# Kernel optimization log

Hardware: AMD Instinct MI355X
Metric: run time of the kernel (lower is better)

The kernel has to match this reference:

```python
import jax, jax.numpy as jnp
import numpy as np

B, D, N, H = 2, 1024, 2048, 16
Da = D // H
NEG = -1e30


def setup_inputs() -> dict:
    key = jax.random.key(0)
    k1, k2, k3, k4, k5 = jax.random.split(key, 5)
    x = jax.random.normal(k1, (B, D, N), dtype=jnp.float32)
    mask = jnp.ones((B, N), dtype=jnp.float32)
    s = 1.0 / np.sqrt(D)
    Wq = jax.random.normal(k2, (H, D, Da), dtype=jnp.float32) * s
    Wk = jax.random.normal(k3, (H, D, Da), dtype=jnp.float32) * s
    Wv = jax.random.normal(k4, (H, D, Da), dtype=jnp.float32) * s
    Wo = jax.random.normal(k5, (D, D), dtype=jnp.float32) * s
    return {"x": x, "mask": mask, "Wq": Wq, "Wk": Wk, "Wv": Wv, "Wo": Wo}


def reference(x, mask, Wq, Wk, Wv, Wo):
    # x: [B, D, N] -> [B, N, D]
    xt = jnp.swapaxes(x, 1, 2)
    scale = 1.0 / np.sqrt(Da)
    # per-head projections, batched over heads: [B, H, N, Da]
    q = jnp.einsum("bnd,hde->bhne", xt, Wq)
    k = jnp.einsum("bnd,hde->bhne", xt, Wk)
    v = jnp.einsum("bnd,hde->bhne", xt, Wv)
    # scaled scores: [B, H, N, N]
    scores = jnp.einsum("bhne,bhme->bhnm", q, k) * scale
    hmask = mask[:, None, None, :]  # additive mask over keys
    vmask = mask[:, None, :, None]  # multiplicative mask over queries
    scores = scores * hmask + (1.0 - hmask) * NEG
    attn = jax.nn.softmax(scores, axis=-1) * vmask
    heads = jnp.einsum("bhnm,bhme->bhne", attn, v)
    # concat heads along feature dim: [B, N, H*Da]
    head = jnp.swapaxes(heads, 1, 2).reshape(xt.shape[0], xt.shape[1], H * Da)
    out = head @ Wo  # [B, N, D]
    return jnp.swapaxes(out, 1, 2)  # [B, D, N]
```

## Files before the change

### kernel.cpp

```cpp
#include <hip/hip_runtime.h>

typedef _Float16 f16;
typedef _Float16 f16x4 __attribute__((ext_vector_type(4)));
typedef _Float16 f16x8 __attribute__((ext_vector_type(8)));
typedef __fp16 fp16x2 __attribute__((ext_vector_type(2)));
typedef float f32x4 __attribute__((ext_vector_type(4)));
typedef float f32x16 __attribute__((ext_vector_type(16)));
typedef int i32x4 __attribute__((ext_vector_type(4)));

#define NEGV (-1e30f)
#define MBASE 10.0f

#if __has_builtin(__builtin_amdgcn_exp2f)
#define EXP2(x) __builtin_amdgcn_exp2f(x)
#else
#define EXP2(x) exp2f(x)
#endif

__device__ __forceinline__ void gload16(const f16* g, f16* l) {
  __builtin_amdgcn_global_load_lds(
      (const __attribute__((address_space(1))) void*)g,
      (__attribute__((address_space(3))) void*)l, 16, 0, 0);
}

__device__ __forceinline__ int pkh(float a, float b) {
  fp16x2 p = __builtin_amdgcn_cvt_pkrtz(a, b);
  return __builtin_bit_cast(int, p);
}

__device__ __forceinline__ void plswap(int& a, int& b) {
#if __has_builtin(__builtin_amdgcn_permlane32_swap)
  auto r = __builtin_amdgcn_permlane32_swap(a, b, false, false);
  a = r[0];
  b = r[1];
#else
  int an = __shfl_xor(b, 32);
  int bn = __shfl_xor(a, 32);
  bool lo = (threadIdx.x & 63) < 32;
  int a2 = lo ? a : an;
  int b2 = lo ? bn : b;
  a = a2;
  b = b2;
#endif
}

__global__ __launch_bounds__(256) void prep_kernel(
    const float* __restrict__ x, const float* __restrict__ Wq,
    const float* __restrict__ Wk, const float* __restrict__ Wv,
    const float* __restrict__ Wo, f16* __restrict__ xt,
    f16* __restrict__ WqkvT, f16* __restrict__ WoT)
{
  __shared__ float t[32][33];
  int tx = threadIdx.x & 31, ty = threadIdx.x >> 5;
  int id = blockIdx.x;
  const float* src;
  f16* dst;
  int a0, b0, sld;
  float sc = 1.0f;
  if (id < 4096) {
    int b = id >> 11, rem = id & 2047;
    a0 = (rem >> 6) * 32;
    b0 = (rem & 63) * 32;
    sld = 2048;
    src = x + (size_t)b * 1024 * 2048;
    dst = xt + (size_t)b * 2048 * 1024;
  } else if (id < 7168) {
    int i = id - 4096;
    a0 = (i & 31) * 32;
    b0 = ((i >> 5) & 1) * 32;
    int z = i >> 6, m = z >> 4, h = z & 15;
    sld = 64;
    src = ((m == 0) ? Wq : (m == 1) ? Wk : Wv) + (size_t)h * 65536;
    sc = (m == 0) ? 0.18033688011112042f : 1.0f;
    dst = WqkvT + (size_t)(m * 1024 + h * 64) * 1024;
  } else {
    int i = id - 7168;
    a0 = (i >> 5) * 32;
    b0 = (i & 31) * 32;
    sld = 1024;
    src = Wo;
    dst = WoT;
  }
#pragma unroll
  for (int i = 0; i < 4; ++i)
    t[ty + 8 * i][tx] = src[(size_t)(a0 + ty + 8 * i) * sld + b0 + tx] * sc;
  __syncthreads();
#pragma unroll
  for (int i = 0; i < 4; ++i)
    dst[(size_t)(b0 + ty + 8 * i) * 1024 + a0 + tx] = (f16)t[tx][ty + 8 * i];
}

template <int BN>
__global__ __launch_bounds__(512, 4) void gemm_f16_kernel(
    const f16* __restrict__ A, const f16* __restrict__ Bt,
    int K, int ldc, long bstride, long cstride,
    f16* __restrict__ Ch, float* __restrict__ Cf,
    const float* __restrict__ rowmask, int mcol0,
    f16* __restrict__ Vt)
{
  const int NACC = BN / 64;
  __shared__ __align__(16) f16 smem[16384];
  f16* As = smem;
  f16* Bs = smem + 8192;

  int tid = threadIdx.x;
  int lane = tid & 63, w = tid >> 6, g = lane >> 4, r = lane & 15;
  int wr = w >> 2, wc = w & 3;

  int nbx = gridDim.x;
  int n = nbx * gridDim.y;
  int flat = blockIdx.y * nbx + blockIdx.x;
  int nf = (flat & 7) * (n >> 3) + (flat >> 3);
  int bx = nf % nbx, by = nf / nbx;

  size_t row0 = (size_t)by * 128;
  size_t col0 = (size_t)bx * BN;
  Bt += (size_t)blockIdx.z * (size_t)bstride;

  int l8 = lane >> 3;
  int sseg = ((lane & 7) ^ l8) * 8;
  int r7 = r & 7;

  f32x4 acc[4][NACC];
#pragma unroll
  for (int m = 0; m < 4; ++m)
#pragma unroll
    for (int nn = 0; nn < NACC; ++nn)
      acc[m][nn] = (f32x4){0.f, 0.f, 0.f, 0.f};

  const f16* Ap = A + (row0 + w * 16 + l8) * (size_t)K + sseg;
  const f16* Bp;
  if (BN == 128)
    Bp = Bt + (col0 + w * 16 + l8) * (size_t)K + sseg;
  else
    Bp = Bt + (col0 + w * 8 + l8) * (size_t)K + sseg;

  for (int k0 = 0; k0 < K; k0 += 64) {
    __syncthreads();
#pragma unroll
    for (int i = 0; i < 2; ++i)
      gload16(Ap + (size_t)i * 8 * K + k0, As + w * 1024 + i * 512);
    if (BN == 128) {
#pragma unroll
      for (int i = 0; i < 2; ++i)
        gload16(Bp + (size_t)i * 8 * K + k0, Bs + w * 1024 + i * 512);
    } else {
      gload16(Bp + k0, Bs + w * 512);
    }
    __syncthreads();
#pragma unroll
    for (int j = 0; j < 2; ++j) {
      f16x8 af[4], bf[NACC];
      int tseg = j * 4 + g;
#pragma unroll
      for (int m = 0; m < 4; ++m)
        af[m] = *(const f16x8*)&As[(wr * 64 + m * 16 + r) * 64 + ((tseg ^ r7) << 3)];
#pragma unroll
      for (int nn = 0; nn < NACC; ++nn) {
        int brow = (BN == 128) ? (wc * 32 + nn * 16 + r) : (wc * 16 + r);
        bf[nn] = *(const f16x8*)&Bs[brow * 64 + ((tseg ^ r7) << 3)];
      }
#pragma unroll
      for (int m = 0; m < 4; ++m)
#pragma unroll
        for (int nn = 0; nn < NACC; ++nn)
          acc[m][nn] = __builtin_amdgcn_mfma_f32_16x16x32_f16(af[m], bf[nn], acc[m][nn], 0, 0, 0);
    }
  }

  if (BN == 128 && Vt && col0 >= 2048) {
    int b = (int)(row0 >> 11);
    int n0 = (int)(row0 & 2047);
    int vcol0 = (int)col0 - 2048;
    __syncthreads();
#pragma unroll
    for (int h2 = 0; h2 < 2; ++h2) {
      if ((wc >> 1) == h2) {
        int wcl = wc & 1;
#pragma unroll
        for (int m = 0; m < 4; ++m)
#pragma unroll
          for (int nn = 0; nn < NACC; ++nn) {
            int cl = wcl * 32 + nn * 16 + r;
            int row = wr * 64 + m * 16 + g * 4;
            int rowp = row ^ ((cl & 7) << 3);
            f16x4 v4 = {(f16)acc[m][nn][0], (f16)acc[m][nn][1],
                        (f16)acc[m][nn][2], (f16)acc[m][nn][3]};
            *(f16x4*)&smem[cl * 128 + rowp] = v4;
          }
      }
      __syncthreads();
#pragma unroll
      for (int ii = 0; ii < 2; ++ii) {
        int chunk = ii * 512 + tid;
        int el = chunk >> 4, seg = chunk & 15;
        int rowp = (seg * 8) ^ ((el & 7) << 3);
        f16x8 v8 = *(const f16x8*)&smem[el * 128 + rowp];
        *(f16x8*)&Vt[(size_t)(b * 1024 + vcol0 + h2 * 64 + el) * 2048 + n0 + seg * 8] = v8;
      }
      __syncthreads();
    }
  } else if (Ch) {
    Ch += (size_t)blockIdx.z * (size_t)cstride;
#pragma unroll
    for (int m = 0; m < 4; ++m)
#pragma unroll
      for (int nn = 0; nn < NACC; ++nn)
#pragma unroll
        for (int q = 0; q < 4; ++q) {
          size_t row = row0 + wr * 64 + m * 16 + g * 4 + q;
          int col = (int)col0 + ((BN == 128) ? (wc * 32 + nn * 16 + r) : (wc * 16 + r));
          float v = acc[m][nn][q];
          if (rowmask && col >= mcol0) v *= rowmask[row];
          Ch[row * (size_t)ldc + col] = (f16)v;
        }
  } else {
    Cf += (size_t)blockIdx.z * (size_t)cstride;
#pragma unroll
    for (int m = 0; m < 4; ++m)
#pragma unroll
      for (int nn = 0; nn < NACC; ++nn)
#pragma unroll
        for (int q = 0; q < 4; ++q) {
          int col = (int)col0 + ((BN == 128) ? (wc * 32 + nn * 16 + r) : (wc * 16 + r));
          Cf[(row0 + wr * 64 + m * 16 + g * 4 + q) * (size_t)ldc + col] = acc[m][nn][q];
        }
  }
}

__global__ __launch_bounds__(512, 4) void attn_kernel(const f16* __restrict__ qk,
                                                      const f16* __restrict__ Vt,
                                                      const float* __restrict__ mask,
                                                      f16* __restrict__ head)
{
  __shared__ __align__(16) f16 smem[32768];
  __shared__ __align__(16) float negc[2048];
  __shared__ __align__(16) float ll[8][32];
  __shared__ __align__(16) float il[4][32];
  __shared__ int aflag;

  int tid = threadIdx.x;
  int w = tid >> 6, lane = tid & 63;
  int l31 = lane & 31, hb = lane >> 5;
  int hb4 = hb * 4;
  int wq = w >> 1, wk = w & 1;

  int flat = blockIdx.x;
  int nf = (flat & 7) * 64 + (flat >> 3);
  int qt = nf & 15, bh = nf >> 4;
  int b = bh >> 4, hh = bh & 15;
  const float* maskb = mask + b * 2048;

  if (tid == 0) aflag = 0;

  int qrow = qt * 128 + wq * 32 + l31;
  const f16* qp = qk + ((size_t)(b * 2048 + qrow)) * 2048 + hh * 64;
  f16x8 qf[4];
#pragma unroll
  for (int ec = 0; ec < 4; ++ec)
    qf[ec] = *(const f16x8*)(qp + ec * 16 + hb * 8);

  const f16* kg0 = qk + ((size_t)(b * 2048)) * 2048 + 1024 + hh * 64;
  const f16* vg0 = Vt + ((size_t)((b * 16 + hh) * 64)) * 2048;

  int ksrow = tid >> 3, kseg = tid & 7;
  int ks2 = (kseg ^ (ksrow & 7)) * 8;
  int vsrow = tid >> 4, vseg2 = tid & 15;
  int vs2 = (vseg2 ^ (vsrow & 7)) * 8;

  auto stage = [&](int nb, int kt_) {
    const f16* kg = kg0 + (size_t)kt_ * 128 * 2048;
    const f16* vg = vg0 + kt_ * 128;
    f16* Kd = smem + nb * 8192;
    f16* Vd = smem + 16384 + nb * 8192;
    gload16(kg + (size_t)ksrow * 2048 + ks2, Kd + w * 512);
    gload16(kg + (size_t)(ksrow + 64) * 2048 + ks2, Kd + 4096 + w * 512);
    gload16(vg + (size_t)vsrow * 2048 + vs2, Vd + w * 512);
    gload16(vg + (size_t)(vsrow + 32) * 2048 + vs2, Vd + 4096 + w * 512);
  };

  stage(0, 0);
  __syncthreads();

  {
    const float* mp = maskb + tid * 4;
    f32x4 m0 = *(const f32x4*)(mp);
    int localany = 0;
#pragma unroll
    for (int j = 0; j < 4; ++j) {
      negc[tid * 4 + j] = (1.0f - m0[j]) * NEGV;
      localany |= (m0[j] != 1.0f);
    }
    if (localany) aflag = 1;
  }
  __syncthreads();
  const bool anymask = (aflag != 0);

  f32x16 zc;
#pragma unroll
  for (int i = 0; i < 16; ++i) zc[i] = 0.f;
  f32x16 o0 = zc, o1 = zc;
  float lrun = 0.f;

  int kb0 = (wk * 64 + l31) * 64;
  int kb1 = kb0 + 2048;
  int k7 = l31 & 7;
  int vb0 = l31 * 128, vb1 = vb0 + 4096;

  for (int kt = 0; kt < 16; ++kt) {
    int cur = kt & 1;
    if (kt + 1 < 16) stage(cur ^ 1, kt + 1);

    const f16* Kc = smem + cur * 8192;
    const f16* Vc = smem + 16384 + cur * 8192;

    f32x16 c0 = zc, c1 = zc;
    if (anymask) {
      const float* nb = &negc[kt * 128 + wk * 64];
#pragma unroll
      for (int rr = 0; rr < 4; ++rr) {
        f32x4 cc0 = *(const f32x4*)&nb[rr * 8 + hb4];
        f32x4 cc1 = *(const f32x4*)&nb[32 + rr * 8 + hb4];
#pragma unroll
        for (int j = 0; j < 4; ++j) {
          c0[rr * 4 + j] = cc0[j];
          c1[rr * 4 + j] = cc1[j];
        }
      }
    }
    f32x16 s0, s1;
    __builtin_amdgcn_s_setprio(1);
    {
      int so = (((hb) ^ k7) << 3);
      f16x8 kf0 = *(const f16x8*)&Kc[kb0 + so];
      f16x8 kf1 = *(const f16x8*)&Kc[kb1 + so];
      s0 = __builtin_amdgcn_mfma_f32_32x32x16_f16(kf0, qf[0], c0, 0, 0, 0);
      s1 = __builtin_amdgcn_mfma_f32_32x32x16_f16(kf1, qf[0], c1, 0, 0, 0);
    }
#pragma unroll
    for (int ec = 1; ec < 4; ++ec) {
      int so = ((((ec << 1) | hb) ^ k7) << 3);
      f16x8 kf0 = *(const f16x8*)&Kc[kb0 + so];
      f16x8 kf1 = *(const f16x8*)&Kc[kb1 + so];
      s0 = __builtin_amdgcn_mfma_f32_32x32x16_f16(kf0, qf[ec], s0, 0, 0, 0);
      s1 = __builtin_amdgcn_mfma_f32_32x32x16_f16(kf1, qf[ec], s1, 0, 0, 0);
    }
    __builtin_amdgcn_s_setprio(0);

    float p[2][16];
#pragma unroll
    for (int i = 0; i < 16; ++i) {
      p[0][i] = EXP2(s0[i] - MBASE);
      p[1][i] = EXP2(s1[i] - MBASE);
    }
    float b2[16];
#pragma unroll
    for (int i = 0; i < 16; ++i) b2[i] = p[0][i] + p[1][i];
#pragma unroll
    for (int stp = 8; stp > 0; stp >>= 1)
#pragma unroll
      for (int i = 0; i < stp; ++i) b2[i] += b2[i + stp];
    lrun += b2[0];

    __builtin_amdgcn_s_setprio(1);
#pragma unroll
    for (int t = 0; t < 2; ++t)
#pragma unroll
      for (int kc = 0; kc < 2; ++kc) {
        int t0a = pkh(p[t][kc * 8 + 0], p[t][kc * 8 + 1]);
        int t0b = pkh(p[t][kc * 8 + 2], p[t][kc * 8 + 3]);
        int t1a = pkh(p[t][kc * 8 + 4], p[t][kc * 8 + 5]);
        int t1b = pkh(p[t][kc * 8 + 6], p[t][kc * 8 + 7]);
        plswap(t0a, t1a);
        plswap(t0b, t1b);
        f16x8 af = __builtin_bit_cast(f16x8, (i32x4){t0a, t0b, t1a, t1b});
        int vseg = wk * 8 + t * 4 + kc * 2 + hb;
        int vs = ((vseg ^ k7) << 3);
        f16x8 vf0 = *(const f16x8*)&Vc[vb0 + vs];
        f16x8 vf1 = *(const f16x8*)&Vc[vb1 + vs];
        o0 = __builtin_amdgcn_mfma_f32_32x32x16_f16(af, vf0, o0, 0, 0, 0);
        o1 = __builtin_amdgcn_mfma_f32_32x32x16_f16(af, vf1, o1, 0, 0, 0);
      }
    __builtin_amdgcn_s_setprio(0);

    __syncthreads();
  }

  lrun += __shfl_xor(lrun, 32);
  if (hb == 0) ll[w][l31] = lrun;
  __syncthreads();
  float lt = lrun + ll[w ^ 1][l31];
  if (wk == 0 && hb == 0) il[wq][l31] = maskb[qrow] / lt;
  float* scr = (float*)smem;
  if (wk == 1) {
    float* sp = scr + wq * 2048;
#pragma unroll
    for (int i = 0; i < 16; ++i) {
      sp[i * 64 + lane] = o0[i];
      sp[(16 + i) * 64 + lane] = o1[i];
    }
  }
  __syncthreads();
  if (wk == 0) {
    float* sp = scr + wq * 2048;
#pragma unroll
    for (int i = 0; i < 16; ++i) {
      o0[i] += sp[i * 64 + lane];
      o1[i] += sp[(16 + i) * 64 + lane];
    }
    f16* hp = head + ((size_t)(b * 2048 + qt * 128 + wq * 32)) * 1024 + hh * 64 + l31;
#pragma unroll
    for (int rr = 0; rr < 4; ++rr) {
      f32x4 iv = *(const f32x4*)&il[wq][rr * 8 + hb4];
#pragma unroll
      for (int j = 0; j < 4; ++j) {
        int crow = j + rr * 8 + hb4;
        hp[(size_t)crow * 1024] = (f16)(o0[rr * 4 + j] * iv[j]);
        hp[(size_t)crow * 1024 + 32] = (f16)(o1[rr * 4 + j] * iv[j]);
      }
    }
  }
}

extern "C" void kernel_launch(void* const* d_in, const int* in_sizes, int n_in,
                              void* d_out, int out_size, void* d_ws, size_t ws_size,
                              hipStream_t stream)
{
  const float* x    = (const float*)d_in[0];
  const float* mask = (const float*)d_in[1];
  const float* Wq   = (const float*)d_in[2];
  const float* Wk   = (const float*)d_in[3];
  const float* Wv   = (const float*)d_in[4];
  const float* Wo   = (const float*)d_in[5];
  float* out = (float*)d_out;

  char* ws = (char*)d_ws;
  f16* xt_head = (f16*)(ws);
  f16* WqkvT   = (f16*)(ws + 8388608);
  f16* WoT     = (f16*)(ws + 14680064);
  f16* qk      = (f16*)(ws + 16777216);
  f16* Vt      = (f16*)(ws + 33554432);

  prep_kernel<<<dim3(8192), 256, 0, stream>>>(x, Wq, Wk, Wv, Wo, xt_head, WqkvT, WoT);

  gemm_f16_kernel<128><<<dim3(24, 32, 1), 512, 0, stream>>>(
      xt_head, WqkvT, 1024, 2048, 0, 0, qk, nullptr, mask, 1024, Vt);

  attn_kernel<<<dim3(512), 512, 0, stream>>>(qk, Vt, mask, xt_head);

  gemm_f16_kernel<64><<<dim3(32, 8, 2), 512, 0, stream>>>(
      WoT, xt_head, 1024, 2048, (long)2048 * 1024, (long)1024 * 2048, nullptr, out,
      nullptr, 0, nullptr);
}
```

Baseline: 117.8 us.

## Halve attention query tile, drop LDS double buffering, split keys across four waves

The attention kernel now processes 64 query rows per block instead of 128, launches twice as many blocks, and splits each 128-key tile across four waves of 32 keys each instead of two waves of 64. K/V staging becomes single-buffered with a sync after each load, and the mask bias is stored as fp16. Together these cut LDS and register use so more blocks fit per CU (launch bounds raised to 8). The cost is that global-to-LDS loads no longer overlap compute, each K/V tile is reloaded by twice as many blocks, and the cross-wave output reduction needs extra LDS round trips. The mask constant changes from -1e30 to -60000 in fp16, which only matters when the mask contains zeros.

```diff
diff --git a/kernel.cpp b/kernel.cpp
--- a/kernel.cpp
+++ b/kernel.cpp
@@ -228,32 +228,45 @@
   }
 }
 
-__global__ __launch_bounds__(512, 4) void attn_kernel(const f16* __restrict__ qk,
+__global__ __launch_bounds__(512, 8) void attn_kernel(const f16* __restrict__ qk,
                                                       const f16* __restrict__ Vt,
                                                       const float* __restrict__ mask,
                                                       f16* __restrict__ head)
 {
-  __shared__ __align__(16) f16 smem[32768];
-  __shared__ __align__(16) float negc[2048];
+  __shared__ __align__(16) f16 smem[16384];
+  __shared__ __align__(16) f16 negcH[2048];
   __shared__ __align__(16) float ll[8][32];
-  __shared__ __align__(16) float il[4][32];
+  __shared__ __align__(16) float il[2][32];
   __shared__ int aflag;
 
   int tid = threadIdx.x;
   int w = tid >> 6, lane = tid & 63;
   int l31 = lane & 31, hb = lane >> 5;
   int hb4 = hb * 4;
-  int wq = w >> 1, wk = w & 1;
+  int wq = w >> 2, wk = w & 3;
 
   int flat = blockIdx.x;
-  int nf = (flat & 7) * 64 + (flat >> 3);
-  int qt = nf & 15, bh = nf >> 4;
+  int nf = (flat & 7) * 128 + (flat >> 3);
+  int qt = nf & 31, bh = nf >> 5;
   int b = bh >> 4, hh = bh & 15;
   const float* maskb = mask + b * 2048;
 
   if (tid == 0) aflag = 0;
-
-  int qrow = qt * 128 + wq * 32 + l31;
+  __syncthreads();
+
+  {
+    const float* mp = maskb + tid * 4;
+    f32x4 m0 = *(const f32x4*)(mp);
+    int localany = 0;
+#pragma unroll
+    for (int j = 0; j < 4; ++j) {
+      negcH[tid * 4 + j] = (f16)((1.0f - m0[j]) * -60000.0f);
+      localany |= (m0[j] != 1.0f);
+    }
+    if (localany) aflag = 1;
+  }
+
+  int qrow = qt * 64 + wq * 32 + l31;
   const f16* qp = qk + ((size_t)(b * 2048 + qrow)) * 2048 + hh * 64;
   f16x8 qf[4];
 #pragma unroll
@@ -268,31 +281,15 @@
   int vsrow = tid >> 4, vseg2 = tid & 15;
   int vs2 = (vseg2 ^ (vsrow & 7)) * 8;
 
-  auto stage = [&](int nb, int kt_) {
+  auto stage = [&](int kt_) {
     const f16* kg = kg0 + (size_t)kt_ * 128 * 2048;
     const f16* vg = vg0 + kt_ * 128;
-    f16* Kd = smem + nb * 8192;
-    f16* Vd = smem + 16384 + nb * 8192;
-    gload16(kg + (size_t)ksrow * 2048 + ks2, Kd + w * 512);
-    gload16(kg + (size_t)(ksrow + 64) * 2048 + ks2, Kd + 4096 + w * 512);
-    gload16(vg + (size_t)vsrow * 2048 + vs2, Vd + w * 512);
-    gload16(vg + (size_t)(vsrow + 32) * 2048 + vs2, Vd + 4096 + w * 512);
+    gload16(kg + (size_t)ksrow * 2048 + ks2, smem + w * 512);
+    gload16(kg + (size_t)(ksrow + 64) * 2048 + ks2, smem + 4096 + w * 512);
+    gload16(vg + (size_t)vsrow * 2048 + vs2, smem + 8192 + w * 512);
+    gload16(vg + (size_t)(vsrow + 32) * 2048 + vs2, smem + 12288 + w * 512);
   };
 
-  stage(0, 0);
-  __syncthreads();
-
-  {
-    const float* mp = maskb + tid * 4;
-    f32x4 m0 = *(const f32x4*)(mp);
-    int localany = 0;
-#pragma unroll
-    for (int j = 0; j < 4; ++j) {
-      negc[tid * 4 + j] = (1.0f - m0[j]) * NEGV;
-      localany |= (m0[j] != 1.0f);
-    }
-    if (localany) aflag = 1;
-  }
   __syncthreads();
   const bool anymask = (aflag != 0);
 
@@ -302,85 +299,63 @@
   f32x16 o0 = zc, o1 = zc;
   float lrun = 0.f;
 
-  int kb0 = (wk * 64 + l31) * 64;
-  int kb1 = kb0 + 2048;
+  int kb0 = (wk * 32 + l31) * 64;
   int k7 = l31 & 7;
   int vb0 = l31 * 128, vb1 = vb0 + 4096;
 
   for (int kt = 0; kt < 16; ++kt) {
-    int cur = kt & 1;
-    if (kt + 1 < 16) stage(cur ^ 1, kt + 1);
-
-    const f16* Kc = smem + cur * 8192;
-    const f16* Vc = smem + 16384 + cur * 8192;
-
-    f32x16 c0 = zc, c1 = zc;
+    stage(kt);
+    __syncthreads();
+
+    const f16* Kc = smem;
+    const f16* Vc = smem + 8192;
+
+    f32x16 s = zc;
     if (anymask) {
-      const float* nb = &negc[kt * 128 + wk * 64];
-#pragma unroll
-      for (int rr = 0; rr < 4; ++rr) {
-        f32x4 cc0 = *(const f32x4*)&nb[rr * 8 + hb4];
-        f32x4 cc1 = *(const f32x4*)&nb[32 + rr * 8 + hb4];
-#pragma unroll
-        for (int j = 0; j < 4; ++j) {
-          c0[rr * 4 + j] = cc0[j];
-          c1[rr * 4 + j] = cc1[j];
-        }
-      }
-    }
-    f32x16 s0, s1;
+      const f16* nb = &negcH[kt * 128 + wk * 32];
+#pragma unroll
+      for (int rr = 0; rr < 4; ++rr)
+#pragma unroll
+        for (int j = 0; j < 4; ++j)
+          s[rr * 4 + j] = (float)nb[rr * 8 + hb4 + j];
+    }
     __builtin_amdgcn_s_setprio(1);
-    {
-      int so = (((hb) ^ k7) << 3);
-      f16x8 kf0 = *(const f16x8*)&Kc[kb0 + so];
-      f16x8 kf1 = *(const f16x8*)&Kc[kb1 + so];
-      s0 = __builtin_amdgcn_mfma_f32_32x32x16_f16(kf0, qf[0], c0, 0, 0, 0);
-      s1 = __builtin_amdgcn_mfma_f32_32x32x16_f16(kf1, qf[0], c1, 0, 0, 0);
-    }
-#pragma unroll
-    for (int ec = 1; ec < 4; ++ec) {
+#pragma unroll
+    for (int ec = 0; ec < 4; ++ec) {
       int so = ((((ec << 1) | hb) ^ k7) << 3);
-      f16x8 kf0 = *(const f16x8*)&Kc[kb0 + so];
-      f16x8 kf1 = *(const f16x8*)&Kc[kb1 + so];
-      s0 = __builtin_amdgcn_mfma_f32_32x32x16_f16(kf0, qf[ec], s0, 0, 0, 0);
-      s1 = __builtin_amdgcn_mfma_f32_32x32x16_f16(kf1, qf[ec], s1, 0, 0, 0);
+      f16x8 kf = *(const f16x8*)&Kc[kb0 + so];
+      s = __builtin_amdgcn_mfma_f32_32x32x16_f16(kf, qf[ec], s, 0, 0, 0);
     }
     __builtin_amdgcn_s_setprio(0);
 
-    float p[2][16];
-#pragma unroll
-    for (int i = 0; i < 16; ++i) {
-      p[0][i] = EXP2(s0[i] - MBASE);
-      p[1][i] = EXP2(s1[i] - MBASE);
-    }
-    float b2[16];
-#pragma unroll
-    for (int i = 0; i < 16; ++i) b2[i] = p[0][i] + p[1][i];
-#pragma unroll
-    for (int stp = 8; stp > 0; stp >>= 1)
+#pragma unroll
+    for (int i = 0; i < 16; ++i) s[i] = EXP2(s[i] - MBASE);
+    float b2[8];
+#pragma unroll
+    for (int i = 0; i < 8; ++i) b2[i] = s[i] + s[i + 8];
+#pragma unroll
+    for (int stp = 4; stp > 0; stp >>= 1)
 #pragma unroll
       for (int i = 0; i < stp; ++i) b2[i] += b2[i + stp];
     lrun += b2[0];
 
     __builtin_amdgcn_s_setprio(1);
 #pragma unroll
-    for (int t = 0; t < 2; ++t)
-#pragma unroll
-      for (int kc = 0; kc < 2; ++kc) {
-        int t0a = pkh(p[t][kc * 8 + 0], p[t][kc * 8 + 1]);
-        int t0b = pkh(p[t][kc * 8 + 2], p[t][kc * 8 + 3]);
-        int t1a = pkh(p[t][kc * 8 + 4], p[t][kc * 8 + 5]);
-        int t1b = pkh(p[t][kc * 8 + 6], p[t][kc * 8 + 7]);
-        plswap(t0a, t1a);
-        plswap(t0b, t1b);
-        f16x8 af = __builtin_bit_cast(f16x8, (i32x4){t0a, t0b, t1a, t1b});
-        int vseg = wk * 8 + t * 4 + kc * 2 + hb;
-        int vs = ((vseg ^ k7) << 3);
-        f16x8 vf0 = *(const f16x8*)&Vc[vb0 + vs];
-        f16x8 vf1 = *(const f16x8*)&Vc[vb1 + vs];
-        o0 = __builtin_amdgcn_mfma_f32_32x32x16_f16(af, vf0, o0, 0, 0, 0);
-        o1 = __builtin_amdgcn_mfma_f32_32x32x16_f16(af, vf1, o1, 0, 0, 0);
-      }
+    for (int kc = 0; kc < 2; ++kc) {
+      int t0a = pkh(s[kc * 8 + 0], s[kc * 8 + 1]);
+      int t0b = pkh(s[kc * 8 + 2], s[kc * 8 + 3]);
+      int t1a = pkh(s[kc * 8 + 4], s[kc * 8 + 5]);
+      int t1b = pkh(s[kc * 8 + 6], s[kc * 8 + 7]);
+      plswap(t0a, t1a);
+      plswap(t0b, t1b);
+      f16x8 af = __builtin_bit_cast(f16x8, (i32x4){t0a, t0b, t1a, t1b});
+      int vseg = wk * 4 + kc * 2 + hb;
+      int vs = ((vseg ^ k7) << 3);
+      f16x8 vf0 = *(const f16x8*)&Vc[vb0 + vs];
+      f16x8 vf1 = *(const f16x8*)&Vc[vb1 + vs];
+      o0 = __builtin_amdgcn_mfma_f32_32x32x16_f16(af, vf0, o0, 0, 0, 0);
+      o1 = __builtin_amdgcn_mfma_f32_32x32x16_f16(af, vf1, o1, 0, 0, 0);
+    }
     __builtin_amdgcn_s_setprio(0);
 
     __syncthreads();
@@ -389,11 +364,13 @@
   lrun += __shfl_xor(lrun, 32);
   if (hb == 0) ll[w][l31] = lrun;
   __syncthreads();
-  float lt = lrun + ll[w ^ 1][l31];
-  if (wk == 0 && hb == 0) il[wq][l31] = maskb[qrow] / lt;
+  if (wk == 0 && hb == 0) {
+    float lt = ll[w][l31] + ll[w + 1][l31] + ll[w + 2][l31] + ll[w + 3][l31];
+    il[wq][l31] = maskb[qrow] / lt;
+  }
   float* scr = (float*)smem;
-  if (wk == 1) {
-    float* sp = scr + wq * 2048;
+  if (wk & 1) {
+    float* sp = scr + (wq * 2 + (wk >> 1)) * 2048;
 #pragma unroll
     for (int i = 0; i < 16; ++i) {
       sp[i * 64 + lane] = o0[i];
@@ -401,14 +378,32 @@
     }
   }
   __syncthreads();
-  if (wk == 0) {
-    float* sp = scr + wq * 2048;
+  if (!(wk & 1)) {
+    float* sp = scr + (wq * 2 + (wk >> 1)) * 2048;
 #pragma unroll
     for (int i = 0; i < 16; ++i) {
       o0[i] += sp[i * 64 + lane];
       o1[i] += sp[(16 + i) * 64 + lane];
     }
-    f16* hp = head + ((size_t)(b * 2048 + qt * 128 + wq * 32)) * 1024 + hh * 64 + l31;
+  }
+  __syncthreads();
+  if (wk == 2) {
+    float* sp = scr + wq * 2048;
+#pragma unroll
+    for (int i = 0; i < 16; ++i) {
+      sp[i * 64 + lane] = o0[i];
+      sp[(16 + i) * 64 + lane] = o1[i];
+    }
+  }
+  __syncthreads();
+  if (wk == 0) {
+    float* sp = scr + wq * 2048;
+#pragma unroll
+    for (int i = 0; i < 16; ++i) {
+      o0[i] += sp[i * 64 + lane];
+      o1[i] += sp[(16 + i) * 64 + lane];
+    }
+    f16* hp = head + ((size_t)(b * 2048 + qt * 64 + wq * 32)) * 1024 + hh * 64 + l31;
 #pragma unroll
     for (int rr = 0; rr < 4; ++rr) {
       f32x4 iv = *(const f32x4*)&il[wq][rr * 8 + hb4];
@@ -446,7 +441,7 @@
   gemm_f16_kernel<128><<<dim3(24, 32, 1), 512, 0, stream>>>(
       xt_head, WqkvT, 1024, 2048, 0, 0, qk, nullptr, mask, 1024, Vt);
 
-  attn_kernel<<<dim3(512), 512, 0, stream>>>(qk, Vt, mask, xt_head);
+  attn_kernel<<<dim3(1024), 512, 0, stream>>>(qk, Vt, mask, xt_head);
 
   gemm_f16_kernel<64><<<dim3(32, 8, 2), 512, 0, stream>>>(
       WoT, xt_head, 1024, 2048, (long)2048 * 1024, (long)1024 * 2048, nullptr, out,
```

New measurement: 203.0 us. 72.3% more time.
